# Performance work log

Measured on AMD Instinct MI355X. Metric: run time of the kernel, lower is better.

The kernel has to match this reference:

```python
import jax, jax.numpy as jnp
import numpy as np

# dims: B=8, T=12, N=512, F_in=64, H=8, F'=out_features//H=8
NEG_SLOPE = 0.01  # torch LeakyReLU default


def setup_inputs() -> dict:
    key = jax.random.key(0)
    ks = jax.random.split(key, 8)
    B, T, N, Fin, H, Fp = 8, 12, 512, 64, 8, 8
    x = jax.random.normal(ks[0], (B, T, N, Fin), dtype=jnp.float32)
    # sparse-ish adjacency with guaranteed self loops (avoids all -inf rows)
    adj = (jax.random.uniform(ks[1], (N, N)) < 0.05).astype(jnp.float32)
    adj = jnp.clip(adj + jnp.eye(N, dtype=jnp.float32), 0.0, 1.0)
    # per-head Linear(in_features, F'): stacked weights [H, Fin, F'] + bias [H, F']
    W = jax.random.normal(ks[2], (H, Fin, Fp), dtype=jnp.float32) * 0.1
    Wb = jax.random.normal(ks[3], (H, Fp), dtype=jnp.float32) * 0.1
    # per-head Linear(2F', 1): split into src-half a1 (multiplies h_j, first F'
    # of the concat) and dst-half a2 (multiplies h_i), plus scalar bias ab
    a1 = jax.random.normal(ks[4], (H, Fp), dtype=jnp.float32) * 0.1
    a2 = jax.random.normal(ks[5], (H, Fp), dtype=jnp.float32) * 0.1
    ab = jax.random.normal(ks[6], (H,), dtype=jnp.float32) * 0.1
    return {"x": x, "adj": adj, "W": W, "Wb": Wb, "a1": a1, "a2": a2, "ab": ab}


def reference(x, adj, W, Wb, a1, a2, ab):
    # h[b,t,h,n,f'] = x @ W_h + b_h
    h = jnp.einsum('btni,hio->bthno', x, W) + Wb[:, None, :]
    # a(cat(h_j, h_i)) = a1.h_j + a2.h_i + ab  (exact decomposition of the
    # original broadcast-concat; avoids the O(N^2 * 2F') a_input tensor)
    s_src = jnp.einsum('bthno,ho->bthn', h, a1)  # contributes along j axis
    s_dst = jnp.einsum('bthno,ho->bthn', h, a2)  # contributes along i axis
    e = jax.nn.leaky_relu(
        s_src[..., None, :] + s_dst[..., :, None] + ab[:, None, None],
        negative_slope=NEG_SLOPE,
    )  # [B,T,H,N,N]
    e = jnp.where(adj == 0, -jnp.inf, e)
    attn = jax.nn.softmax(e, axis=-1)  # (dropout is identity in eval mode)
    h_prime = jnp.einsum('bthij,bthjo->bthio', attn, h)  # [B,T,H,N,F']
    B, T, H, N, Fp = h_prime.shape
    # concat heads along feature dim, matching torch.cat(head_outputs, -1)
    return h_prime.transpose(0, 1, 3, 2, 4).reshape(B, T, N, H * Fp)
```

## Files before the change

### kernel.cpp

```cpp
#include <hip/hip_runtime.h>
#include <math.h>

namespace {

constexpr int kN    = 512;
constexpr int kFin  = 64;
constexpr int kH    = 8;
constexpr int kFp   = 8;
constexpr int kBT   = 96;
constexpr int kNT   = 256;
constexpr int kMaxDeg = 104;
constexpr float kNeg = 0.01f;
constexpr float kL2E = 1.44269504088896340736f;

typedef _Float16 half8t __attribute__((ext_vector_type(8)));
typedef unsigned int uint;

__device__ __forceinline__ float fast_exp2(float v) {
#if __has_builtin(__builtin_amdgcn_exp2f)
  return __builtin_amdgcn_exp2f(v);
#else
  return exp2f(v);
#endif
}

constexpr int kOffBits = 0;
constexpr int kOffPerm = kOffBits + kN * 16;
constexpr int kOffDeg  = kOffPerm + kN;
constexpr int kOffIdx  = kOffDeg + kN;

__global__ void pack_adj_kernel(const float* __restrict__ adj,
                                uint* __restrict__ bitsR) {
  const int t = blockIdx.x * blockDim.x + threadIdx.x;
  const unsigned long long m = __ballot(adj[t] != 0.0f);
  const int lane = threadIdx.x & 63;
  if ((lane & 31) == 0) {
    const int i = t >> 9;
    const int w = (t & 511) >> 5;
    bitsR[i * 16 + w] = (uint)(m >> (lane & 32));
  }
}

__global__ __launch_bounds__(64) void rank_fill_kernel(
    const uint* __restrict__ bitsR, uint* __restrict__ permG,
    uint* __restrict__ degG, uint* __restrict__ idxG) {
  __shared__ int degS[kN];
  const int i = blockIdx.x;
  const int l = threadIdx.x;

#pragma unroll
  for (int r8 = 0; r8 < 8; ++r8) {
    const int r = l + r8 * 64;
    const uint4* p = reinterpret_cast<const uint4*>(&bitsR[r * 16]);
    const uint4 a = p[0], b = p[1], c = p[2], d = p[3];
    degS[r] = __popc(a.x) + __popc(a.y) + __popc(a.z) + __popc(a.w) +
              __popc(b.x) + __popc(b.y) + __popc(b.z) + __popc(b.w) +
              __popc(c.x) + __popc(c.y) + __popc(c.z) + __popc(c.w) +
              __popc(d.x) + __popc(d.y) + __popc(d.z) + __popc(d.w);
  }
  __syncthreads();

  const int degi = degS[i];
  int cnt = 0;
#pragma unroll
  for (int r8 = 0; r8 < 8; ++r8) {
    const int r = l + r8 * 64;
    const int dr = degS[r];
    cnt += (dr < degi || (dr == degi && r < i)) ? 1 : 0;
  }
#pragma unroll
  for (int off = 32; off > 0; off >>= 1) cnt += __shfl_xor(cnt, off, 64);
  const int pos = cnt;
  if (l == 0) {
    permG[pos] = (uint)i;
    degG[pos] = (uint)degi;
  }

  uint b = (l < 16) ? bitsR[i * 16 + l] : 0u;
  const int cntw = __popc(b);
  int scan = cntw;
#pragma unroll
  for (int off = 1; off < 16; off <<= 1) {
    const int v = __shfl_up(scan, off, 64);
    if (l >= off) scan += v;
  }
  int slot = scan - cntw;
  while (b) {
    const int j = l * 32 + __builtin_ctz(b);
    b &= b - 1;
    idxG[slot * kN + pos] = (uint)j;
    ++slot;
  }
}

__global__ __launch_bounds__(kNT) void gat_sparse_kernel(
    const float* __restrict__ x, const uint* __restrict__ permG,
    const uint* __restrict__ degG, const uint* __restrict__ idxG,
    const float* __restrict__ W, const float* __restrict__ Wb,
    const float* __restrict__ a1, const float* __restrict__ a2,
    const float* __restrict__ ab, float* __restrict__ out) {
  __shared__ _Float16 h16S[kN * 8];
  __shared__ float ssrcS[kN];
  __shared__ float sdstS[kN];

  const int bt  = blockIdx.x % kBT;
  const int h   = blockIdx.x / kBT;
  const int tid = threadIdx.x;

  const int p0 = 2 * tid;
  const uint2 ip = *reinterpret_cast<const uint2*>(&permG[p0]);
  const uint2 dp = *reinterpret_cast<const uint2*>(&degG[p0]);
  uint2 jj = *reinterpret_cast<const uint2*>(&idxG[p0]);

  const float* xb = x + (size_t)bt * kN * kFin;
  const float* Wl = W + h * kFin * kFp;

  float xr0[kFin], xr1[kFin];
  {
    const float4* px0 = reinterpret_cast<const float4*>(xb + (size_t)tid * kFin);
    const float4* px1 =
        reinterpret_cast<const float4*>(xb + (size_t)(tid + kNT) * kFin);
#pragma unroll
    for (int c4 = 0; c4 < kFin / 4; ++c4) {
      *reinterpret_cast<float4*>(&xr0[c4 * 4]) = px0[c4];
      *reinterpret_cast<float4*>(&xr1[c4 * 4]) = px1[c4];
    }
  }

  float acc0[kFp], acc1[kFp];
#pragma unroll
  for (int f = 0; f < kFp; ++f) {
    const float b = Wb[h * kFp + f];
    acc0[f] = b;
    acc1[f] = b;
  }
#pragma unroll
  for (int i = 0; i < kFin; ++i) {
#pragma unroll
    for (int f = 0; f < kFp; ++f) {
      const float wv = Wl[i * kFp + f];
      acc0[f] = fmaf(xr0[i], wv, acc0[f]);
      acc1[f] = fmaf(xr1[i], wv, acc1[f]);
    }
  }

  float s1a = 0.f, s2a = 0.f, s1b = 0.f, s2b = 0.f;
#pragma unroll
  for (int f = 0; f < kFp; ++f) {
    const float A1 = a1[h * kFp + f];
    const float A2 = a2[h * kFp + f];
    s1a = fmaf(acc0[f], A1, s1a);
    s2a = fmaf(acc0[f], A2, s2a);
    s1b = fmaf(acc1[f], A1, s1b);
    s2b = fmaf(acc1[f], A2, s2b);
  }
  const float abh = ab[h];
  ssrcS[tid]       = s1a * kL2E;
  ssrcS[tid + kNT] = s1b * kL2E;
  sdstS[tid]       = (s2a + abh) * kL2E;
  sdstS[tid + kNT] = (s2b + abh) * kL2E;

  {
    half8t hv;
#pragma unroll
    for (int f = 0; f < kFp; ++f) hv[f] = (_Float16)acc0[f];
    *reinterpret_cast<half8t*>(&h16S[(size_t)tid * 8]) = hv;
#pragma unroll
    for (int f = 0; f < kFp; ++f) hv[f] = (_Float16)acc1[f];
    *reinterpret_cast<half8t*>(&h16S[(size_t)(tid + kNT) * 8]) = hv;
  }
  __syncthreads();

  const int i0 = (int)ip.x, i1 = (int)ip.y;
  const int d0 = (int)dp.x, d1 = (int)dp.y;
  const float sd0 = sdstS[i0];
  const float sd1 = sdstS[i1];
  const int dmax = max(d0, d1);

  float o0[kFp], o1[kFp];
#pragma unroll
  for (int f = 0; f < kFp; ++f) {
    o0[f] = 0.f;
    o1[f] = 0.f;
  }
  float sum0 = 0.f, sum1 = 0.f;

#pragma unroll 1
  for (int slot = 0; slot < dmax; ++slot) {
    const uint2 jn =
        *reinterpret_cast<const uint2*>(&idxG[(slot + 1) * kN + p0]);
    const int j0 = (int)(jj.x & 511u);
    const int j1 = (int)(jj.y & 511u);

    const half8t hv0 = *reinterpret_cast<const half8t*>(&h16S[(size_t)j0 * 8]);
    const half8t hv1 = *reinterpret_cast<const half8t*>(&h16S[(size_t)j1 * 8]);
    float e0 = ssrcS[j0] + sd0;
    float e1 = ssrcS[j1] + sd1;
    e0 = fmaxf(e0, e0 * kNeg);
    e1 = fmaxf(e1, e1 * kNeg);
    float q0 = fast_exp2(e0);
    float q1 = fast_exp2(e1);
    q0 = (slot < d0) ? q0 : 0.f;
    q1 = (slot < d1) ? q1 : 0.f;
    sum0 += q0;
    sum1 += q1;
#pragma unroll
    for (int f = 0; f < kFp; ++f) {
      o0[f] = fmaf((float)hv0[f], q0, o0[f]);
      o1[f] = fmaf((float)hv1[f], q1, o1[f]);
    }
    jj = jn;
  }

  const float r0 = 1.0f / sum0;
  const float r1 = 1.0f / sum1;
  float* q0p = out + (((size_t)bt * kN + i0) * kH + h) * kFp;
  float* q1p = out + (((size_t)bt * kN + i1) * kH + h) * kFp;
  reinterpret_cast<float4*>(q0p)[0] =
      make_float4(o0[0] * r0, o0[1] * r0, o0[2] * r0, o0[3] * r0);
  reinterpret_cast<float4*>(q0p)[1] =
      make_float4(o0[4] * r0, o0[5] * r0, o0[6] * r0, o0[7] * r0);
  reinterpret_cast<float4*>(q1p)[0] =
      make_float4(o1[0] * r1, o1[1] * r1, o1[2] * r1, o1[3] * r1);
  reinterpret_cast<float4*>(q1p)[1] =
      make_float4(o1[4] * r1, o1[5] * r1, o1[6] * r1, o1[7] * r1);
}

}

extern "C" void kernel_launch(void* const* d_in, const int* in_sizes, int n_in,
                              void* d_out, int out_size, void* d_ws, size_t ws_size,
                              hipStream_t stream) {
  const float* x   = (const float*)d_in[0];
  const float* adj = (const float*)d_in[1];
  const float* W   = (const float*)d_in[2];
  const float* Wb  = (const float*)d_in[3];
  const float* a1  = (const float*)d_in[4];
  const float* a2  = (const float*)d_in[5];
  const float* ab  = (const float*)d_in[6];
  float* out = (float*)d_out;

  uint* ws    = (uint*)d_ws;
  uint* bitsR = ws + kOffBits;
  uint* permG = ws + kOffPerm;
  uint* degG  = ws + kOffDeg;
  uint* idxG  = ws + kOffIdx;

  hipLaunchKernelGGL(pack_adj_kernel, dim3(kN * kN / kNT), dim3(kNT), 0, stream,
                     adj, bitsR);
  hipLaunchKernelGGL(rank_fill_kernel, dim3(kN), dim3(64), 0, stream,
                     bitsR, permG, degG, idxG);
  hipLaunchKernelGGL(gat_sparse_kernel, dim3(kBT * kH), dim3(kNT), 0, stream,
                     x, permG, degG, idxG, W, Wb, a1, a2, ab, out);
}
```

Measured before the change: 103.5 us.

## Fuse adjacency packing, ranking and GAT into one persistent kernel with grid barriers

Merges the three kernels (adjacency bit-packing, degree ranking/index fill, sparse attention) into one kernel of 768 blocks that uses two software grid barriers built from atomic counters, which are zeroed by a memset before launch. Adjacency packing is spread across all blocks and overlaps with the feature projection. This is meant to remove the launch gaps and serial tail between the small preprocessing kernels. It relies on all 768 blocks being co-resident (launch_bounds min 3 blocks/CU), otherwise it deadlocks, and it adds a memset launch plus spin-wait cost.

Measured after the change: 266.3 us. +157.4%, slower.

```diff
diff --git a/kernel.cpp b/kernel.cpp
--- a/kernel.cpp
+++ b/kernel.cpp
@@ -28,92 +28,57 @@
 constexpr int kOffPerm = kOffBits + kN * 16;
 constexpr int kOffDeg  = kOffPerm + kN;
 constexpr int kOffIdx  = kOffDeg + kN;
-
-__global__ void pack_adj_kernel(const float* __restrict__ adj,
-                                uint* __restrict__ bitsR) {
-  const int t = blockIdx.x * blockDim.x + threadIdx.x;
-  const unsigned long long m = __ballot(adj[t] != 0.0f);
-  const int lane = threadIdx.x & 63;
-  if ((lane & 31) == 0) {
-    const int i = t >> 9;
-    const int w = (t & 511) >> 5;
-    bitsR[i * 16 + w] = (uint)(m >> (lane & 32));
-  }
-}
-
-__global__ __launch_bounds__(64) void rank_fill_kernel(
-    const uint* __restrict__ bitsR, uint* __restrict__ permG,
-    uint* __restrict__ degG, uint* __restrict__ idxG) {
-  __shared__ int degS[kN];
-  const int i = blockIdx.x;
-  const int l = threadIdx.x;
-
-#pragma unroll
-  for (int r8 = 0; r8 < 8; ++r8) {
-    const int r = l + r8 * 64;
-    const uint4* p = reinterpret_cast<const uint4*>(&bitsR[r * 16]);
-    const uint4 a = p[0], b = p[1], c = p[2], d = p[3];
-    degS[r] = __popc(a.x) + __popc(a.y) + __popc(a.z) + __popc(a.w) +
-              __popc(b.x) + __popc(b.y) + __popc(b.z) + __popc(b.w) +
-              __popc(c.x) + __popc(c.y) + __popc(c.z) + __popc(c.w) +
-              __popc(d.x) + __popc(d.y) + __popc(d.z) + __popc(d.w);
-  }
+constexpr int kOffCnt  = kOffIdx + kMaxDeg * kN;
+
+__device__ __forceinline__ void grid_barrier(uint* cnt, uint target) {
   __syncthreads();
-
-  const int degi = degS[i];
-  int cnt = 0;
-#pragma unroll
-  for (int r8 = 0; r8 < 8; ++r8) {
-    const int r = l + r8 * 64;
-    const int dr = degS[r];
-    cnt += (dr < degi || (dr == degi && r < i)) ? 1 : 0;
-  }
-#pragma unroll
-  for (int off = 32; off > 0; off >>= 1) cnt += __shfl_xor(cnt, off, 64);
-  const int pos = cnt;
-  if (l == 0) {
-    permG[pos] = (uint)i;
-    degG[pos] = (uint)degi;
-  }
-
-  uint b = (l < 16) ? bitsR[i * 16 + l] : 0u;
-  const int cntw = __popc(b);
-  int scan = cntw;
-#pragma unroll
-  for (int off = 1; off < 16; off <<= 1) {
-    const int v = __shfl_up(scan, off, 64);
-    if (l >= off) scan += v;
-  }
-  int slot = scan - cntw;
-  while (b) {
-    const int j = l * 32 + __builtin_ctz(b);
-    b &= b - 1;
-    idxG[slot * kN + pos] = (uint)j;
-    ++slot;
-  }
-}
-
-__global__ __launch_bounds__(kNT) void gat_sparse_kernel(
-    const float* __restrict__ x, const uint* __restrict__ permG,
-    const uint* __restrict__ degG, const uint* __restrict__ idxG,
+  if (threadIdx.x == 0) {
+    __threadfence();
+    atomicAdd(cnt, 1u);
+    while (__hip_atomic_load(cnt, __ATOMIC_RELAXED,
+                             __HIP_MEMORY_SCOPE_AGENT) < target) {
+      __builtin_amdgcn_s_sleep(2);
+    }
+    __threadfence();
+  }
+  __syncthreads();
+}
+
+__global__ __launch_bounds__(kNT, 3) void gat_mega(
+    const float* __restrict__ x, const float* __restrict__ adj,
     const float* __restrict__ W, const float* __restrict__ Wb,
     const float* __restrict__ a1, const float* __restrict__ a2,
-    const float* __restrict__ ab, float* __restrict__ out) {
+    const float* __restrict__ ab, float* __restrict__ out,
+    uint* __restrict__ ws) {
   __shared__ _Float16 h16S[kN * 8];
   __shared__ float ssrcS[kN];
   __shared__ float sdstS[kN];
-
-  const int bt  = blockIdx.x % kBT;
-  const int h   = blockIdx.x / kBT;
+  __shared__ int degS[kN];
+
+  uint* bitsR = ws + kOffBits;
+  uint* permG = ws + kOffPerm;
+  uint* degG  = ws + kOffDeg;
+  uint* idxG  = ws + kOffIdx;
+  uint* cnts  = ws + kOffCnt;
+
+  const int blk = blockIdx.x;
   const int tid = threadIdx.x;
-
-  const int p0 = 2 * tid;
-  const uint2 ip = *reinterpret_cast<const uint2*>(&permG[p0]);
-  const uint2 dp = *reinterpret_cast<const uint2*>(&degG[p0]);
-  uint2 jj = *reinterpret_cast<const uint2*>(&idxG[p0]);
+  const int bt  = blk % kBT;
+  const int h   = blk / kBT;
 
   const float* xb = x + (size_t)bt * kN * kFin;
   const float* Wl = W + h * kFin * kFp;
+
+  {
+    const int stride = kBT * kH * kNT;
+    for (int e = blk * kNT + tid; e < kN * kN; e += stride) {
+      const unsigned long long m = __ballot(adj[e] != 0.0f);
+      const int lane = tid & 63;
+      if ((lane & 31) == 0) {
+        bitsR[(e >> 9) * 16 + ((e & 511) >> 5)] = (uint)(m >> (lane & 32));
+      }
+    }
+  }
 
   float xr0[kFin], xr1[kFin];
   {
@@ -169,7 +134,63 @@
     for (int f = 0; f < kFp; ++f) hv[f] = (_Float16)acc1[f];
     *reinterpret_cast<half8t*>(&h16S[(size_t)(tid + kNT) * 8]) = hv;
   }
-  __syncthreads();
+
+  grid_barrier(&cnts[0], (uint)(kBT * kH));
+
+  if (blk < kN) {
+#pragma unroll
+    for (int rr = 0; rr < 2; ++rr) {
+      const int r = tid + rr * kNT;
+      const uint4* p = reinterpret_cast<const uint4*>(&bitsR[r * 16]);
+      const uint4 a = p[0], b4 = p[1], c = p[2], d = p[3];
+      degS[r] = __popc(a.x) + __popc(a.y) + __popc(a.z) + __popc(a.w) +
+                __popc(b4.x) + __popc(b4.y) + __popc(b4.z) + __popc(b4.w) +
+                __popc(c.x) + __popc(c.y) + __popc(c.z) + __popc(c.w) +
+                __popc(d.x) + __popc(d.y) + __popc(d.z) + __popc(d.w);
+    }
+    __syncthreads();
+    if (tid < 64) {
+      const int i = blk;
+      const int l = tid;
+      const int degi = degS[i];
+      int cntv = 0;
+#pragma unroll
+      for (int r8 = 0; r8 < 8; ++r8) {
+        const int r = l + r8 * 64;
+        const int dr = degS[r];
+        cntv += (dr < degi || (dr == degi && r < i)) ? 1 : 0;
+      }
+#pragma unroll
+      for (int off = 32; off > 0; off >>= 1) cntv += __shfl_xor(cntv, off, 64);
+      const int pos = cntv;
+      if (l == 0) {
+        permG[pos] = (uint)i;
+        degG[pos] = (uint)degi;
+      }
+      uint b = (l < 16) ? bitsR[i * 16 + l] : 0u;
+      const int cw = __popc(b);
+      int scan = cw;
+#pragma unroll
+      for (int off = 1; off < 16; off <<= 1) {
+        const int v = __shfl_up(scan, off, 64);
+        if (l >= off) scan += v;
+      }
+      int slot = scan - cw;
+      while (b) {
+        const int j = l * 32 + __builtin_ctz(b);
+        b &= b - 1;
+        idxG[slot * kN + pos] = (uint)j;
+        ++slot;
+      }
+    }
+  }
+
+  grid_barrier(&cnts[1], (uint)(kBT * kH));
+
+  const int p0 = 2 * tid;
+  const uint2 ip = *reinterpret_cast<const uint2*>(&permG[p0]);
+  const uint2 dp = *reinterpret_cast<const uint2*>(&degG[p0]);
+  uint2 jj = *reinterpret_cast<const uint2*>(&idxG[p0]);
 
   const int i0 = (int)ip.x, i1 = (int)ip.y;
   const int d0 = (int)dp.x, d1 = (int)dp.y;
@@ -239,17 +260,10 @@
   const float* a2  = (const float*)d_in[5];
   const float* ab  = (const float*)d_in[6];
   float* out = (float*)d_out;
-
-  uint* ws    = (uint*)d_ws;
-  uint* bitsR = ws + kOffBits;
-  uint* permG = ws + kOffPerm;
-  uint* degG  = ws + kOffDeg;
-  uint* idxG  = ws + kOffIdx;
-
-  hipLaunchKernelGGL(pack_adj_kernel, dim3(kN * kN / kNT), dim3(kNT), 0, stream,
-                     adj, bitsR);
-  hipLaunchKernelGGL(rank_fill_kernel, dim3(kN), dim3(64), 0, stream,
-                     bitsR, permG, degG, idxG);
-  hipLaunchKernelGGL(gat_sparse_kernel, dim3(kBT * kH), dim3(kNT), 0, stream,
-                     x, permG, degG, idxG, W, Wb, a1, a2, ab, out);
-}
+  uint* ws   = (uint*)d_ws;
+
+  hipMemsetAsync((char*)d_ws + (size_t)kOffCnt * sizeof(uint), 0,
+                 2 * sizeof(uint), stream);
+  hipLaunchKernelGGL(gat_mega, dim3(kBT * kH), dim3(kNT), 0, stream,
+                     x, adj, W, Wb, a1, a2, ab, out, ws);
+}
```
